# Optimization experiments

Hardware: AMD Instinct MI355X
Metric: run time of the kernel (lower is better)

The kernel has to match this reference:

```python
import jax, jax.numpy as jnp
import numpy as np

D_MODEL = 1024
NUM_HEADS = 16
D_K = D_MODEL // NUM_HEADS  # 64
THETA = 10000.0
B, S = 2, 2048


def _rope(x, cos, sin):
    # x: [b, h, s, d]; cos/sin: [s, d//2] (broadcast over b, h)
    x1 = x[..., 0::2]
    x2 = x[..., 1::2]
    y1 = x1 * cos - x2 * sin
    y2 = x1 * sin + x2 * cos
    # interleave back: stack on last dim then flatten pairs
    return jnp.stack([y1, y2], axis=-1).reshape(x.shape)


def setup_inputs() -> dict:
    key = jax.random.key(0)
    ks = jax.random.split(key, 5)
    scale = 1.0 / np.sqrt(D_MODEL)
    return {
        "x": jax.random.normal(ks[0], (B, S, D_MODEL), dtype=jnp.float32),
        "token_positions": jnp.arange(S, dtype=jnp.int32),
        "Wq": jax.random.normal(ks[1], (D_MODEL, D_MODEL), dtype=jnp.float32) * scale,
        "Wk": jax.random.normal(ks[2], (D_MODEL, D_MODEL), dtype=jnp.float32) * scale,
        "Wv": jax.random.normal(ks[3], (D_MODEL, D_MODEL), dtype=jnp.float32) * scale,
        "Wo": jax.random.normal(ks[4], (D_MODEL, D_MODEL), dtype=jnp.float32) * scale,
    }


def reference(x, token_positions, Wq, Wk, Wv, Wo):
    b, s, _ = x.shape
    # torch nn.Linear semantics (no bias in this repo's Linear): y = x @ W.T
    q = jnp.einsum("bsd,od->bso", x, Wq)
    k = jnp.einsum("bsd,od->bso", x, Wk)
    v = jnp.einsum("bsd,od->bso", x, Wv)
    # split heads: b s (h d) -> b h s d
    def split(t):
        return t.reshape(b, s, NUM_HEADS, D_K).transpose(0, 2, 1, 3)
    q, k, v = split(q), split(k), split(v)

    # RoPE tables
    inv_freq = 1.0 / (THETA ** (jnp.arange(0, D_K, 2, dtype=jnp.float32) / D_K))  # [d/2]
    freqs = token_positions.astype(jnp.float32)[:, None] * inv_freq[None, :]      # [s, d/2]
    cos, sin = jnp.cos(freqs), jnp.sin(freqs)
    q = _rope(q, cos, sin)
    k = _rope(k, cos, sin)

    scale = D_K ** (-0.5)
    scores = jnp.einsum("bhqd,bhkd->bhqk", q, k) * scale  # [b,h,s,s]
    causal = jnp.tril(jnp.ones((s, s), dtype=bool))
    scores = jnp.where(causal, scores, -jnp.inf)
    attn = jax.nn.softmax(scores, axis=-1)
    out = jnp.einsum("bhqk,bhkd->bhqd", attn, v)
    out = out.transpose(0, 2, 1, 3).reshape(b, s, D_MODEL)  # b h s d -> b s (h d)
    return jnp.einsum("bsd,od->bso", out, Wo)
```

## Files before the change

kernel.cpp:

```cpp
#include <hip/hip_runtime.h>
#include <hip/hip_bf16.h>
#include <math.h>

#define SS 2048

typedef __attribute__((ext_vector_type(8))) __bf16 bf16x8;
typedef __attribute__((ext_vector_type(4))) float f32x4;
typedef __attribute__((ext_vector_type(16))) float f32x16;
typedef __attribute__((ext_vector_type(4))) unsigned int u32x4;
typedef __attribute__((ext_vector_type(4))) unsigned short u16x4;

__device__ __forceinline__ f32x4 mfma16(bf16x8 a, bf16x8 b, f32x4 c) {
  return __builtin_amdgcn_mfma_f32_16x16x32_bf16(a, b, c, 0, 0, 0);
}
__device__ __forceinline__ f32x16 mfma32(bf16x8 a, bf16x8 b, f32x16 c) {
  return __builtin_amdgcn_mfma_f32_32x32x16_bf16(a, b, c, 0, 0, 0);
}

__device__ __forceinline__ void gld_lds16(const void* g, void* l) {
  __builtin_amdgcn_global_load_lds(
      (__attribute__((address_space(1))) void*)(g),
      (__attribute__((address_space(3))) void*)(l), 16, 0, 0);
}

#if __has_builtin(__builtin_amdgcn_exp2f)
#define EXP2F(x) __builtin_amdgcn_exp2f(x)
#else
#define EXP2F(x) __expf(0.69314718056f * (x))
#endif

__device__ __forceinline__ unsigned int cvtpk_bf16(float lo, float hi) {
  unsigned int r;
  asm("v_cvt_pk_bf16_f32 %0, %1, %2" : "=v"(r) : "v"(lo), "v"(hi));
  return r;
}
__device__ __forceinline__ void swap32(unsigned int& x, unsigned int& y) {
  asm("v_permlane32_swap_b32 %0, %1" : "+v"(x), "+v"(y));
}
__device__ __forceinline__ unsigned short bfu(float v) {
  __bf16 h = (__bf16)v;
  return __builtin_bit_cast(unsigned short, h);
}

__global__ void prep_kernel(const float* __restrict__ x, const float* __restrict__ Wq,
                            const float* __restrict__ Wk, const float* __restrict__ Wv,
                            const float* __restrict__ Wo, const int* __restrict__ pos,
                            __bf16* __restrict__ xb, __bf16* __restrict__ Wb,
                            float2* __restrict__ tab) {
  const int bid = blockIdx.x, tid = threadIdx.x;
  if (bid >= 4096) {
    int i = (bid - 4096) * 256 + tid;
    int s = i >> 5, j = i & 31;
    float p = (float)pos[s];
    float inv = exp2f((float)j * -0.41524101186098283f);
    float f = p * inv;
    float sn, cs;
    sincosf(f, &sn, &cs);
    tab[i] = make_float2(cs, sn);
    return;
  }
  const float* s;
  __bf16* d;
  size_t base;
  if (bid < 2048) { s = x; d = xb; base = bid; }
  else {
    int seg = (bid - 2048) >> 9;
    s = (seg == 0) ? Wq : (seg == 1) ? Wk : (seg == 2) ? Wv : Wo;
    d = Wb + (size_t)seg * 1024 * 1024;
    base = (bid - 2048) & 511;
  }
  size_t i = (base * 256 + tid) * 8;
  float4 a = *reinterpret_cast<const float4*>(s + i);
  float4 b = *reinterpret_cast<const float4*>(s + i + 4);
  bf16x8 o;
  o[0] = (__bf16)a.x; o[1] = (__bf16)a.y; o[2] = (__bf16)a.z; o[3] = (__bf16)a.w;
  o[4] = (__bf16)b.x; o[5] = (__bf16)b.y; o[6] = (__bf16)b.z; o[7] = (__bf16)b.w;
  *reinterpret_cast<bf16x8*>(d + i) = o;
}

__global__ __launch_bounds__(512, 1) void gemm256_kernel(
    const __bf16* __restrict__ A, const __bf16* __restrict__ Bw,
    __bf16* __restrict__ C, __bf16* __restrict__ Vt,
    const float2* __restrict__ tab) {
  const int K = 1024, N = 3072, nk = 32;
  __shared__ __align__(16) __bf16 sm[57344];
  __bf16* lsA = sm;
  __bf16* lsB = sm + 32768;

  const int tid = threadIdx.x;
  const int lane = tid & 63;
  const int wave = tid >> 6;
  const int wr = wave >> 2, wc = wave & 3;
  const bool lowW = wave < 6;

  const int xcd = blockIdx.x & 7;
  const int ii = blockIdx.x >> 3;
  const int m0 = (2 * xcd + (ii & 1)) * 256;
  const int n0 = (ii >> 1) * 192;

  const f32x4 fzero = {0.f, 0.f, 0.f, 0.f};
  f32x4 acc[8][3];
#pragma unroll
  for (int f = 0; f < 8; ++f)
#pragma unroll
    for (int g = 0; g < 3; ++g) acc[f][g] = fzero;

  const int arow0 = tid >> 2, ac = tid & 3;
  const __bf16* gA0 = A + (size_t)(m0 + arow0) * K + 8 * (ac ^ ((arow0 >> 1) & 3));
  const __bf16* gA1 = A + (size_t)(m0 + 128 + arow0) * K + 8 * (ac ^ (((arow0 + 128) >> 1) & 3));
  const int bid0 = tid, bid1 = tid + 384;
  const int br0 = bid0 >> 2, br1 = bid1 >> 2;
  const __bf16* gB0 = Bw + (size_t)(n0 + br0) * K + 8 * ((bid0 & 3) ^ ((br0 >> 1) & 3));
  const __bf16* gB1 = Bw + (size_t)(n0 + br1) * K + 8 * ((bid1 & 3) ^ ((br1 >> 1) & 3));

#define STAGE256(kt_)                                                \
  do {                                                               \
    const int kc_ = (kt_) & 3;                                       \
    const int ko_ = (kt_) * 32;                                      \
    gld_lds16(gA0 + ko_, lsA + kc_ * 8192 + tid * 8);                \
    gld_lds16(gA1 + ko_, lsA + kc_ * 8192 + 4096 + tid * 8);         \
    if (lowW) {                                                      \
      gld_lds16(gB0 + ko_, lsB + kc_ * 6144 + tid * 8);              \
      gld_lds16(gB1 + ko_, lsB + kc_ * 6144 + 3072 + tid * 8);       \
    }                                                                \
  } while (0)

  STAGE256(0);
  STAGE256(1);

  const int lrow = lane & 15, hi = lane >> 4;

#pragma unroll 1
  for (int kt = 0; kt < nk; ++kt) {
    const int ksA = (kt & 3) * 8192, ksB = (kt & 3) * 6144;
    if (kt + 2 < nk) {
      STAGE256(kt + 2);
      if (lowW) asm volatile("s_waitcnt vmcnt(8)" ::: "memory");
      else      asm volatile("s_waitcnt vmcnt(4)" ::: "memory");
    } else if (kt == nk - 2) {
      if (lowW) asm volatile("s_waitcnt vmcnt(4)" ::: "memory");
      else      asm volatile("s_waitcnt vmcnt(2)" ::: "memory");
    } else {
      asm volatile("s_waitcnt vmcnt(0)" ::: "memory");
    }
    __builtin_amdgcn_s_barrier();

    bf16x8 bfr[3];
#pragma unroll
    for (int g = 0; g < 3; ++g) {
      const int r = wc * 48 + g * 16 + lrow;
      bfr[g] = *reinterpret_cast<const bf16x8*>(
          lsB + ksB + r * 32 + ((hi ^ ((r >> 1) & 3)) * 8));
    }
    bf16x8 af[4];
#pragma unroll
    for (int f = 0; f < 4; ++f) {
      const int r = wr * 128 + f * 16 + lrow;
      af[f] = *reinterpret_cast<const bf16x8*>(
          lsA + ksA + r * 32 + ((hi ^ ((r >> 1) & 3)) * 8));
    }
    __builtin_amdgcn_s_setprio(1);
#pragma unroll
    for (int f = 0; f < 4; ++f)
#pragma unroll
      for (int g = 0; g < 3; ++g) acc[f][g] = mfma16(af[f], bfr[g], acc[f][g]);
    __builtin_amdgcn_s_setprio(0);
#pragma unroll
    for (int f = 0; f < 4; ++f) {
      const int r = wr * 128 + (f + 4) * 16 + lrow;
      af[f] = *reinterpret_cast<const bf16x8*>(
          lsA + ksA + r * 32 + ((hi ^ ((r >> 1) & 3)) * 8));
    }
    __builtin_amdgcn_s_setprio(1);
#pragma unroll
    for (int f = 0; f < 4; ++f)
#pragma unroll
      for (int g = 0; g < 3; ++g) acc[f + 4][g] = mfma16(af[f], bfr[g], acc[f + 4][g]);
    __builtin_amdgcn_s_setprio(0);
  }
#undef STAGE256

  const int crow = (lane >> 4) * 4, ccol = lane & 15;
  const int par = ccol & 1;
#pragma unroll
  for (int g = 0; g < 3; ++g) {
    const int cb = n0 + wc * 48 + g * 16;
    if (cb < 2048) {
      const int jj = ((cb + ccol) >> 1) & 31;
#pragma unroll
      for (int f = 0; f < 8; ++f) {
#pragma unroll
        for (int t = 0; t < 4; ++t) {
          const int r = m0 + wr * 128 + f * 16 + crow + t;
          const int s = r & (SS - 1);
          float2 cs = tab[(s << 5) | jj];
          float v = acc[f][g][t];
          float o = __shfl_xor(v, 1);
          float y = par ? fmaf(o, cs.y, v * cs.x) : fmaf(v, cs.x, -o * cs.y);
          C[(size_t)r * N + cb + ccol] = (__bf16)y;
        }
      }
    } else {
      const int c = cb - 2048 + ccol;
      const int hh = c >> 6, dd = c & 63;
#pragma unroll
      for (int f = 0; f < 8; ++f) {
        const int r0 = m0 + wr * 128 + f * 16 + crow;
        const int bb = r0 >> 11, s0 = r0 & (SS - 1);
        u16x4 pk;
#pragma unroll
        for (int t = 0; t < 4; ++t) pk[t] = bfu(acc[f][g][t]);
        *reinterpret_cast<u16x4*>(Vt + ((size_t)(bb * 16 + hh) * 64 + dd) * SS + s0) = pk;
      }
    }
  }
}

__global__ __launch_bounds__(512, 1) void gemm_out_kernel(
    const __bf16* __restrict__ A, const __bf16* __restrict__ Bw,
    float* __restrict__ C) {
  const int K = 1024, N = 1024, nk = 32;
  __shared__ __align__(16) __bf16 sm[32768];
  __bf16* lsA = sm;
  __bf16* lsB = sm + 16384;

  const int tid = threadIdx.x;
  const int lane = tid & 63;
  const int wave = tid >> 6;
  const int wr = wave >> 2, wc = wave & 3;

  const int xcd = blockIdx.x & 7;
  const int ii = blockIdx.x >> 3;
  const int m0 = (4 * xcd + (ii & 3)) * 128;
  const int n0 = (ii >> 2) * 128;

  const f32x4 fzero = {0.f, 0.f, 0.f, 0.f};
  f32x4 acc[4][2];
#pragma unroll
  for (int f = 0; f < 4; ++f)
#pragma unroll
    for (int g = 0; g < 2; ++g) acc[f][g] = fzero;

  const int srow = tid >> 2, sc = tid & 3;
  const int ssc = 8 * (sc ^ ((srow >> 1) & 3));
  const __bf16* gA = A + (size_t)(m0 + srow) * K + ssc;
  const __bf16* gB = Bw + (size_t)(n0 + srow) * K + ssc;

#define STAGEO(kt_)                                        \
  do {                                                     \
    const int kc_ = (kt_) & 3;                             \
    gld_lds16(gA + (kt_) * 32, lsA + kc_ * 4096 + tid * 8);\
    gld_lds16(gB + (kt_) * 32, lsB + kc_ * 4096 + tid * 8);\
  } while (0)

  STAGEO(0);
  STAGEO(1);

  const int lrow = lane & 15, hi = lane >> 4;

#pragma unroll 1
  for (int kt = 0; kt < nk; ++kt) {
    const int ks = (kt & 3) * 4096;
    if (kt + 2 < nk) {
      STAGEO(kt + 2);
      asm volatile("s_waitcnt vmcnt(4)" ::: "memory");
    } else if (kt == nk - 2) {
      asm volatile("s_waitcnt vmcnt(2)" ::: "memory");
    } else {
      asm volatile("s_waitcnt vmcnt(0)" ::: "memory");
    }
    __builtin_amdgcn_s_barrier();

    bf16x8 bfr[2], af[4];
#pragma unroll
    for (int g = 0; g < 2; ++g) {
      const int r = wc * 32 + g * 16 + lrow;
      bfr[g] = *reinterpret_cast<const bf16x8*>(
          lsB + ks + r * 32 + ((hi ^ ((r >> 1) & 3)) * 8));
    }
#pragma unroll
    for (int f = 0; f < 4; ++f) {
      const int r = wr * 64 + f * 16 + lrow;
      af[f] = *reinterpret_cast<const bf16x8*>(
          lsA + ks + r * 32 + ((hi ^ ((r >> 1) & 3)) * 8));
    }
    __builtin_amdgcn_s_setprio(1);
#pragma unroll
    for (int f = 0; f < 4; ++f)
#pragma unroll
      for (int g = 0; g < 2; ++g) acc[f][g] = mfma16(af[f], bfr[g], acc[f][g]);
    __builtin_amdgcn_s_setprio(0);
  }
#undef STAGEO

  const int crow = (lane >> 4) * 4, ccol = lane & 15;
#pragma unroll
  for (int f = 0; f < 4; ++f) {
#pragma unroll
    for (int g = 0; g < 2; ++g) {
      int r = m0 + wr * 64 + f * 16 + crow;
      int c = n0 + wc * 32 + g * 16 + ccol;
#pragma unroll
      for (int t = 0; t < 4; ++t) C[(size_t)(r + t) * N + c] = acc[f][g][t];
    }
  }
}

#define CEXP 0.18033688011112042f
#define SHIFT_B 16.0f

#define EXPSUM(S0, S1, L)                                                   \
  {                                                                         \
    float a0_ = 0.f, a1_ = 0.f, a2_ = 0.f, a3_ = 0.f;                       \
    _Pragma("unroll") for (int r = 0; r < 16; r += 4) {                     \
      S0[r] = EXP2F(fmaf(S0[r], CEXP, -SHIFT_B)); a0_ += S0[r];             \
      S0[r + 1] = EXP2F(fmaf(S0[r + 1], CEXP, -SHIFT_B)); a1_ += S0[r + 1]; \
      S0[r + 2] = EXP2F(fmaf(S0[r + 2], CEXP, -SHIFT_B)); a2_ += S0[r + 2]; \
      S0[r + 3] = EXP2F(fmaf(S0[r + 3], CEXP, -SHIFT_B)); a3_ += S0[r + 3]; \
    }                                                                       \
    _Pragma("unroll") for (int r = 0; r < 16; r += 4) {                     \
      S1[r] = EXP2F(fmaf(S1[r], CEXP, -SHIFT_B)); a0_ += S1[r];             \
      S1[r + 1] = EXP2F(fmaf(S1[r + 1], CEXP, -SHIFT_B)); a1_ += S1[r + 1]; \
      S1[r + 2] = EXP2F(fmaf(S1[r + 2], CEXP, -SHIFT_B)); a2_ += S1[r + 2]; \
      S1[r + 3] = EXP2F(fmaf(S1[r + 3], CEXP, -SHIFT_B)); a3_ += S1[r + 3]; \
    }                                                                       \
    float rs_ = (a0_ + a1_) + (a2_ + a3_);                                  \
    rs_ += __shfl_xor(rs_, 32);                                             \
    L += rs_;                                                               \
  }

template <int SPLIT>
__global__ __launch_bounds__(128) void attn_kernel(const __bf16* __restrict__ qkv,
                                                   const __bf16* __restrict__ Vt,
                                                   __bf16* __restrict__ pA,
                                                   __bf16* __restrict__ pB,
                                                   float* __restrict__ pL) {
  const int bid = blockIdx.x;
  const int x = bid & 7, t8 = bid >> 3;
  const int low = t8 & 7, phi = (t8 >> 3) & 3, g = (t8 >> 5) & 3;
  const int half = SPLIT ? (t8 >> 7) : 0;
  const int hp = phi * 8 + x;
  const int b = hp >> 4, h = hp & 15;
  const int qt = (g == 0) ? low : (g == 1) ? 31 - low : (g == 2) ? 15 - low : 16 + low;

  const int nkt = qt + 1;
  const int mid = (nkt + 1) >> 1;
  const int k0 = SPLIT ? (half ? mid : 0) : 0;
  const int k1 = SPLIT ? (half ? nkt : mid) : nkt;

  const int tid = threadIdx.x;
  const int wave = tid >> 6, lane = tid & 63;
  const int q32 = lane & 31, hi = lane >> 5;
  const int qw0 = qt * 64 + wave * 32;
  const int q = qw0 + q32;

  __shared__ __align__(16) __bf16 smem[8192];

  bf16x8 qb[4];
  {
    const __bf16* qr = qkv + (size_t)(b * SS + q) * 3072 + h * 64;
#pragma unroll
    for (int slot = 0; slot < 4; ++slot)
      qb[slot] = *reinterpret_cast<const bf16x8*>(qr + slot * 16 + hi * 8);
  }

  const __bf16* kbase = qkv + (size_t)(b * SS) * 3072 + 1024 + h * 64;
  const __bf16* vbase = Vt + (size_t)((b * 16 + h) * 64) * SS;

  const int srow = tid >> 3, scg = tid & 7;
  const int ssc = 8 * (scg ^ (srow & 7));
  const __bf16* kG0 = kbase + (size_t)srow * 3072 + ssc;
  const __bf16* vG0 = vbase + (size_t)srow * SS + ssc;

  const f32x16 fz16 = {0,0,0,0,0,0,0,0,0,0,0,0,0,0,0,0};
  f32x16 o0 = fz16, o1 = fz16;
  float lsum = 0.f;

#pragma unroll 1
  for (int kt = k0; kt < k1; ++kt) {
    {
      const __bf16* kG = kG0 + (size_t)kt * 64 * 3072;
      const __bf16* vG = vG0 + (size_t)kt * 64;
#pragma unroll
      for (int u = 0; u < 4; ++u)
        gld_lds16(kG + (size_t)u * 16 * 3072, smem + tid * 8 + u * 1024);
#pragma unroll
      for (int u = 0; u < 4; ++u)
        gld_lds16(vG + (size_t)u * 16 * SS, smem + 4096 + tid * 8 + u * 1024);
    }
    asm volatile("s_waitcnt vmcnt(0)" ::: "memory");
    __builtin_amdgcn_s_barrier();

    f32x16 s0 = fz16, s1 = fz16;
    __builtin_amdgcn_s_setprio(1);
#pragma unroll
    for (int slot = 0; slot < 4; ++slot) {
      const int swz = 8 * ((slot * 2 + hi) ^ (q32 & 7));
      bf16x8 kf0 = *reinterpret_cast<const bf16x8*>(smem + q32 * 64 + swz);
      bf16x8 kf1 = *reinterpret_cast<const bf16x8*>(smem + (32 + q32) * 64 + swz);
      s0 = mfma32(kf0, qb[slot], s0);
      s1 = mfma32(kf1, qb[slot], s1);
    }
    __builtin_amdgcn_s_setprio(0);

    if (kt == qt) {
      const int kvb = kt * 64;
#pragma unroll
      for (int r = 0; r < 16; ++r) {
        const int rowc = (r & 3) + 8 * (r >> 2) + 4 * hi;
        if (kvb + rowc > q) s0[r] = -INFINITY;
        if (kvb + 32 + rowc > q) s1[r] = -INFINITY;
      }
    }

    EXPSUM(s0, s1, lsum)

    bf16x8 pb[4];
    {
      unsigned int A = cvtpk_bf16(s0[0], s0[1]), B2 = cvtpk_bf16(s0[2], s0[3]);
      unsigned int C2 = cvtpk_bf16(s0[4], s0[5]), D2 = cvtpk_bf16(s0[6], s0[7]);
      swap32(A, C2); swap32(B2, D2);
      u32x4 t0 = {A, B2, C2, D2};
      pb[0] = __builtin_bit_cast(bf16x8, t0);
      unsigned int E = cvtpk_bf16(s0[8], s0[9]), F = cvtpk_bf16(s0[10], s0[11]);
      unsigned int G = cvtpk_bf16(s0[12], s0[13]), H = cvtpk_bf16(s0[14], s0[15]);
      swap32(E, G); swap32(F, H);
      u32x4 t1 = {E, F, G, H};
      pb[1] = __builtin_bit_cast(bf16x8, t1);
      unsigned int A3 = cvtpk_bf16(s1[0], s1[1]), B3 = cvtpk_bf16(s1[2], s1[3]);
      unsigned int C3 = cvtpk_bf16(s1[4], s1[5]), D3 = cvtpk_bf16(s1[6], s1[7]);
      swap32(A3, C3); swap32(B3, D3);
      u32x4 t2 = {A3, B3, C3, D3};
      pb[2] = __builtin_bit_cast(bf16x8, t2);
      unsigned int E3 = cvtpk_bf16(s1[8], s1[9]), F3 = cvtpk_bf16(s1[10], s1[11]);
      unsigned int G3 = cvtpk_bf16(s1[12], s1[13]), H3 = cvtpk_bf16(s1[14], s1[15]);
      swap32(E3, G3); swap32(F3, H3);
      u32x4 t3 = {E3, F3, G3, H3};
      pb[3] = __builtin_bit_cast(bf16x8, t3);
    }

    __builtin_amdgcn_s_setprio(1);
#pragma unroll
    for (int slot = 0; slot < 4; ++slot) {
      const int swz = 8 * ((slot * 2 + hi) ^ (q32 & 7));
      bf16x8 v0 = *reinterpret_cast<const bf16x8*>(smem + 4096 + q32 * 64 + swz);
      bf16x8 v1 = *reinterpret_cast<const bf16x8*>(smem + 4096 + (32 + q32) * 64 + swz);
      o0 = mfma32(v0, pb[slot], o0);
      o1 = mfma32(v1, pb[slot], o1);
    }
    __builtin_amdgcn_s_setprio(0);

    __builtin_amdgcn_s_barrier();
  }

  const float inv = SPLIT ? 1.0f : (1.0f / lsum);
  __bf16* ol = smem + wave * 2304;
#pragma unroll
  for (int r = 0; r < 16; ++r) {
    const int d = (r & 3) + 8 * (r >> 2) + 4 * hi;
    if (SPLIT) {
      ol[q32 * 72 + d] = (__bf16)o0[r];
      ol[q32 * 72 + 32 + d] = (__bf16)o1[r];
    } else {
      ol[q32 * 72 + d] = (__bf16)(o0[r] * inv);
      ol[q32 * 72 + 32 + d] = (__bf16)(o1[r] * inv);
    }
  }
  __bf16* dst = (SPLIT && half) ? pB : pA;
#pragma unroll
  for (int pass = 0; pass < 4; ++pass) {
    const int idx = pass * 64 + lane;
    const int row = idx >> 3, colc = idx & 7;
    bf16x8 v = *reinterpret_cast<const bf16x8*>(ol + row * 72 + colc * 8);
    *reinterpret_cast<bf16x8*>(
        dst + (size_t)(b * SS + qt * 64 + wave * 32 + row) * 1024 + h * 64 + colc * 8) = v;
  }
  if (SPLIT && hi == 0)
    pL[half * 65536 + hp * 2048 + qt * 64 + wave * 32 + q32] = lsum;
}

__global__ void combine_kernel(const __bf16* __restrict__ pB,
                               const float* __restrict__ pL,
                               __bf16* __restrict__ ao) {
  const int i = (blockIdx.x * 256 + threadIdx.x) * 8;
  const int row = i >> 10, col = i & 1023;
  const int bb = row >> 11, s = row & 2047, h = col >> 6;
  const int bh = bb * 16 + h;
  const float lA = pL[bh * 2048 + s];
  const float lB = pL[65536 + bh * 2048 + s];
  const float inv = 1.0f / (lA + lB);
  bf16x8 a = *reinterpret_cast<const bf16x8*>(ao + i);
  bf16x8 b8 = *reinterpret_cast<const bf16x8*>(pB + i);
  bf16x8 o;
#pragma unroll
  for (int j = 0; j < 8; ++j) o[j] = (__bf16)(((float)a[j] + (float)b8[j]) * inv);
  *reinterpret_cast<bf16x8*>(ao + i) = o;
}

extern "C" void kernel_launch(void* const* d_in, const int* in_sizes, int n_in,
                              void* d_out, int out_size, void* d_ws, size_t ws_size,
                              hipStream_t stream) {
  const float* x  = (const float*)d_in[0];
  const int* pos  = (const int*)d_in[1];
  const float* Wq = (const float*)d_in[2];
  const float* Wk = (const float*)d_in[3];
  const float* Wv = (const float*)d_in[4];
  const float* Wo = (const float*)d_in[5];

  __bf16* xb  = (__bf16*)d_ws;
  __bf16* Wb  = xb + (size_t)4096 * 1024;
  __bf16* qkv = Wb + (size_t)4096 * 1024;
  __bf16* Vt  = qkv + (size_t)4096 * 3072;
  __bf16* ao  = Vt + (size_t)2048 * 2048;
  float2* tab = (float2*)(ao + (size_t)4096 * 1024);
  __bf16* pB  = (__bf16*)(tab + 2048 * 32);
  float*  pL  = (float*)(pB + (size_t)4096 * 1024);

  const size_t NEED = (size_t)(pL + 2 * 32 * 2048) - (size_t)d_ws;

  prep_kernel<<<4352, 256, 0, stream>>>(x, Wq, Wk, Wv, Wo, pos, xb, Wb, tab);
  gemm256_kernel<<<256, 512, 0, stream>>>(xb, Wb, qkv, Vt, tab);
  if (ws_size >= NEED) {
    attn_kernel<1><<<2048, 128, 0, stream>>>(qkv, Vt, ao, pB, pL);
    combine_kernel<<<2048, 256, 0, stream>>>(pB, pL, ao);
  } else {
    attn_kernel<0><<<1024, 128, 0, stream>>>(qkv, Vt, ao, nullptr, nullptr);
  }
  gemm_out_kernel<<<256, 512, 0, stream>>>(ao, Wb + (size_t)3 * 1024 * 1024, (float*)d_out);
}
```

Measured before the change: 104.7 us.

## Double-buffer K/V tiles in LDS to overlap global loads with attention MFMA

The attention loop now uses two LDS buffers and prefetches the next K/V tile with async global-to-LDS loads while the current tile is being computed. Partial vmcnt waits replace the full drain each iteration. The goal is to hide global memory latency behind the QK and PV matrix multiplies. In exchange, LDS use per block doubles, which may lower occupancy.

```diff
diff --git a/kernel.cpp b/kernel.cpp
--- a/kernel.cpp
+++ b/kernel.cpp
@@ -354,7 +354,7 @@
   const int qw0 = qt * 64 + wave * 32;
   const int q = qw0 + q32;
 
-  __shared__ __align__(16) __bf16 smem[8192];
+  __shared__ __align__(16) __bf16 smem[16384];
 
   bf16x8 qb[4];
   {
@@ -363,6 +363,7 @@
     for (int slot = 0; slot < 4; ++slot)
       qb[slot] = *reinterpret_cast<const bf16x8*>(qr + slot * 16 + hi * 8);
   }
+  asm volatile("s_waitcnt vmcnt(0)" ::: "memory");
 
   const __bf16* kbase = qkv + (size_t)(b * SS) * 3072 + 1024 + h * 64;
   const __bf16* vbase = Vt + (size_t)((b * 16 + h) * 64) * SS;
@@ -372,32 +373,44 @@
   const __bf16* kG0 = kbase + (size_t)srow * 3072 + ssc;
   const __bf16* vG0 = vbase + (size_t)srow * SS + ssc;
 
+#define STAGE(buf_, kt_)                                                      \
+  do {                                                                        \
+    const __bf16* kG = kG0 + (size_t)(kt_)*64 * 3072;                         \
+    const __bf16* vG = vG0 + (size_t)(kt_)*64;                                \
+    __bf16* sl_ = smem + (buf_)*8192;                                         \
+    _Pragma("unroll") for (int u = 0; u < 4; ++u) {                           \
+      gld_lds16(kG + (size_t)u * 16 * 3072, sl_ + tid * 8 + u * 1024);        \
+      gld_lds16(vG + (size_t)u * 16 * SS, sl_ + 4096 + tid * 8 + u * 1024);   \
+    }                                                                         \
+  } while (0)
+
   const f32x16 fz16 = {0,0,0,0,0,0,0,0,0,0,0,0,0,0,0,0};
   f32x16 o0 = fz16, o1 = fz16;
   float lsum = 0.f;
 
+  if (k0 < k1) STAGE(0, k0);
+
 #pragma unroll 1
   for (int kt = k0; kt < k1; ++kt) {
-    {
-      const __bf16* kG = kG0 + (size_t)kt * 64 * 3072;
-      const __bf16* vG = vG0 + (size_t)kt * 64;
-#pragma unroll
-      for (int u = 0; u < 4; ++u)
-        gld_lds16(kG + (size_t)u * 16 * 3072, smem + tid * 8 + u * 1024);
-#pragma unroll
-      for (int u = 0; u < 4; ++u)
-        gld_lds16(vG + (size_t)u * 16 * SS, smem + 4096 + tid * 8 + u * 1024);
-    }
-    asm volatile("s_waitcnt vmcnt(0)" ::: "memory");
+    const int buf = (kt - k0) & 1;
+    if (kt + 1 < k1) {
+      STAGE(buf ^ 1, kt + 1);
+      asm volatile("s_waitcnt vmcnt(8)" ::: "memory");
+    } else {
+      asm volatile("s_waitcnt vmcnt(0)" ::: "memory");
+    }
     __builtin_amdgcn_s_barrier();
+
+    const __bf16* lk = smem + buf * 8192;
+    const __bf16* lv = lk + 4096;
 
     f32x16 s0 = fz16, s1 = fz16;
     __builtin_amdgcn_s_setprio(1);
 #pragma unroll
     for (int slot = 0; slot < 4; ++slot) {
       const int swz = 8 * ((slot * 2 + hi) ^ (q32 & 7));
-      bf16x8 kf0 = *reinterpret_cast<const bf16x8*>(smem + q32 * 64 + swz);
-      bf16x8 kf1 = *reinterpret_cast<const bf16x8*>(smem + (32 + q32) * 64 + swz);
+      bf16x8 kf0 = *reinterpret_cast<const bf16x8*>(lk + q32 * 64 + swz);
+      bf16x8 kf1 = *reinterpret_cast<const bf16x8*>(lk + (32 + q32) * 64 + swz);
       s0 = mfma32(kf0, qb[slot], s0);
       s1 = mfma32(kf1, qb[slot], s1);
     }
@@ -443,8 +456,8 @@
 #pragma unroll
     for (int slot = 0; slot < 4; ++slot) {
       const int swz = 8 * ((slot * 2 + hi) ^ (q32 & 7));
-      bf16x8 v0 = *reinterpret_cast<const bf16x8*>(smem + 4096 + q32 * 64 + swz);
-      bf16x8 v1 = *reinterpret_cast<const bf16x8*>(smem + 4096 + (32 + q32) * 64 + swz);
+      bf16x8 v0 = *reinterpret_cast<const bf16x8*>(lv + q32 * 64 + swz);
+      bf16x8 v1 = *reinterpret_cast<const bf16x8*>(lv + (32 + q32) * 64 + swz);
       o0 = mfma32(v0, pb[slot], o0);
       o1 = mfma32(v1, pb[slot], o1);
     }
@@ -452,6 +465,9 @@
 
     __builtin_amdgcn_s_barrier();
   }
+
+  asm volatile("s_waitcnt vmcnt(0)" ::: "memory");
+  __builtin_amdgcn_s_barrier();
 
   const float inv = SPLIT ? 1.0f : (1.0f / lsum);
   __bf16* ol = smem + wave * 2304;
```

Result: slower. 113.0 us (+7.9%).
